# Kernel tuning notes

Hardware: AMD Instinct MI355X
Metric: run time of the kernel (lower is better)

Reference implementation:

```python
import jax, jax.numpy as jnp
import numpy as np

T, H = 4096, 2048

def setup_inputs() -> dict:
    key = jax.random.key(0)
    k1, k2, k3 = jax.random.split(key, 3)
    x_sequence = jax.random.normal(k1, (T, H), dtype=jnp.float32)
    lamda = jax.random.normal(k2, (H,), dtype=jnp.float32) * 0.2
    B = jax.random.normal(k3, (H, H), dtype=jnp.float32) / jnp.sqrt(jnp.float32(H))
    return {"x_sequence": x_sequence, "lamda": lamda, "B": B}

def reference(x_sequence, lamda, B):
    # h_t = lamda \odot h_{t-1} + B @ x_t ; initial h_0 = 0 (reset_rtrl_state).
    # Returns stacked h over all T steps, matching torch.stack(outputs).
    def step(h, x_t):
        h_next = lamda * h + B @ x_t  # [H]
        return h_next, h_next
    h0 = jnp.zeros_like(lamda)
    _, hs = jax.lax.scan(step, h0, x_sequence)  # hs: [T, H]
    return hs
```

## Files before the change

kernel.cpp:

```cpp
#include <hip/hip_runtime.h>
#include <hip/hip_bf16.h>

#define T_DIM 4096
#define H_DIM 2048
#define K_DIM 2048
#define NCHUNK 64
#define CLEN 64
#define NT (K_DIM / 64)

typedef float f32x4 __attribute__((ext_vector_type(4)));
typedef _Float16 f16x8 __attribute__((ext_vector_type(8)));

typedef const __attribute__((address_space(1))) char* gp1;
typedef __attribute__((address_space(3))) char* lp3;

static const size_t nX = (size_t)T_DIM * K_DIM;
static const size_t nB = (size_t)H_DIM * K_DIM;

__global__ __launch_bounds__(256) void cvt_swz_all(const float* __restrict__ X,
                                                   const float* __restrict__ Bm,
                                                   _Float16* __restrict__ Xh,
                                                   _Float16* __restrict__ Bh) {
    size_t i = ((size_t)blockIdx.x * 256 + threadIdx.x) * 8;
    const float* in;
    _Float16* out;
    size_t j;
    if (i < nX) { in = X;  out = Xh; j = i; }
    else        { in = Bm; out = Bh; j = i - nX; }
    int row  = (int)(j >> 11);
    int colB = (int)(j & 2047) * 2;
    float a[8];
    *(f32x4*)(a)     = *(const f32x4*)(in + j);
    *(f32x4*)(a + 4) = *(const f32x4*)(in + j + 4);
    f16x8 h;
#pragma unroll
    for (int k = 0; k < 8; ++k) h[k] = (_Float16)a[k];
    size_t ob = (size_t)row * 4096 + (size_t)(colB ^ ((row & 7) << 4));
    *(f16x8*)((char*)out + ob) = h;
}

__global__ __launch_bounds__(512) void gemm_f16(const _Float16* __restrict__ Xh,
                                                const _Float16* __restrict__ Bh,
                                                const float* __restrict__ lamda,
                                                float* __restrict__ Y,
                                                float* __restrict__ e) {
    __shared__ __align__(16) _Float16 sA[2][128 * 64];
    __shared__ __align__(16) _Float16 sB[2][128 * 64];

    int bid = blockIdx.x;
    int swz = (bid & 7) * 64 + (bid >> 3);
    const int h0 = (swz & 15) * 128;
    const int t0 = (swz >> 4) * 128;

    const int tid  = threadIdx.x;
    const int lane = tid & 63;
    const int wave = tid >> 6;
    const int wrow = wave >> 2;
    const int wcol = wave & 3;
    const int ln15 = lane & 15;
    const int kq   = lane >> 4;

    f32x4 acc[4][2] = {};

    const int srow = tid >> 3;
    const int kcB  = (tid & 7) * 16;
    size_t gA0[2], gB0[2];
    unsigned ldsOff[2];
#pragma unroll
    for (int q = 0; q < 2; ++q) {
        gA0[q] = (size_t)(t0 + srow + q * 64) * 4096 + kcB;
        gB0[q] = (size_t)(h0 + srow + q * 64) * 4096 + kcB;
        ldsOff[q] = (unsigned)((q * 512 + wave * 64) * 16);
    }

    int baseA[4], swzA[4], baseB[2], swzB[2];
#pragma unroll
    for (int m = 0; m < 4; ++m) {
        int rA = wrow * 64 + m * 16 + ln15;
        baseA[m] = rA * 128; swzA[m] = (rA & 7) << 4;
    }
#pragma unroll
    for (int n = 0; n < 2; ++n) {
        int rB = wcol * 32 + n * 16 + ln15;
        baseB[n] = rB * 128; swzB[n] = (rB & 7) << 4;
    }

#define STAGE(buf, kt)                                                                   \
    {                                                                                    \
        _Pragma("unroll")                                                                \
        for (int q = 0; q < 2; ++q) {                                                    \
            __builtin_amdgcn_global_load_lds((gp1)((const char*)Xh + gA0[q] + (kt) * 128), \
                                             (lp3)((char*)sA[buf] + ldsOff[q]), 16, 0, 0); \
            __builtin_amdgcn_global_load_lds((gp1)((const char*)Bh + gB0[q] + (kt) * 128), \
                                             (lp3)((char*)sB[buf] + ldsOff[q]), 16, 0, 0); \
        }                                                                                \
    }

#define COMPUTE(buf)                                                                     \
    {                                                                                    \
        const char* pA = (const char*)sA[buf];                                           \
        const char* pB = (const char*)sB[buf];                                           \
        _Pragma("unroll")                                                                \
        for (int kk = 0; kk < 2; ++kk) {                                                 \
            const int kb = kk * 64 + kq * 16;                                            \
            f16x8 fa[4], fb[2];                                                          \
            _Pragma("unroll")                                                            \
            for (int m = 0; m < 4; ++m)                                                  \
                fa[m] = *(const f16x8*)(pA + baseA[m] + (kb ^ swzA[m]));                 \
            _Pragma("unroll")                                                            \
            for (int n = 0; n < 2; ++n)                                                  \
                fb[n] = *(const f16x8*)(pB + baseB[n] + (kb ^ swzB[n]));                 \
            _Pragma("unroll")                                                            \
            for (int m = 0; m < 4; ++m)                                                  \
                _Pragma("unroll")                                                        \
                for (int n = 0; n < 2; ++n)                                              \
                    acc[m][n] = __builtin_amdgcn_mfma_f32_16x16x32_f16(fa[m], fb[n],     \
                                                                      acc[m][n], 0, 0, 0); \
        }                                                                                \
    }

    STAGE(0, 0);
    __syncthreads();

    int cur = 0;
    for (int kt = 0; kt < NT; ++kt) {
        if (kt + 1 < NT) STAGE(cur ^ 1, kt + 1);
        COMPUTE(cur);
        __syncthreads();
        cur ^= 1;
    }
#undef STAGE
#undef COMPUTE

#pragma unroll
    for (int m = 0; m < 4; ++m) {
        int row = t0 + wrow * 64 + m * 16 + kq * 4;
#pragma unroll
        for (int n = 0; n < 2; ++n) {
            int col = h0 + wcol * 32 + n * 16 + ln15;
#pragma unroll
            for (int j = 0; j < 4; ++j)
                Y[(size_t)(row + j) * H_DIM + col] = acc[m][n][j];
        }
    }

    const int c = (t0 >> 6) + wrow;
#pragma unroll
    for (int n = 0; n < 2; ++n) {
        int col = h0 + wcol * 32 + n * 16 + ln15;
        float lam  = lamda[col];
        float lam2 = lam * lam;
        float lam4 = lam2 * lam2;
        float lam16 = lam4 * lam4 * lam4 * lam4;
        float hsum = 0.f;
#pragma unroll
        for (int m = 0; m < 4; ++m) {
            float hm = fmaf(fmaf(fmaf(acc[m][n][0], lam, acc[m][n][1]), lam,
                                 acc[m][n][2]), lam, acc[m][n][3]);
            hsum = fmaf(hsum, lam16, hm);
        }
        float w = 1.f;
        if (kq < 3) w = lam4;
        if (kq < 2) w *= lam4;
        if (kq < 1) w *= lam4;
        float T = hsum * w;
        T += __shfl_xor(T, 16);
        T += __shfl_xor(T, 32);
        if (kq == 0) e[(size_t)c * H_DIM + col] = T;
    }
}

__global__ __launch_bounds__(256) void scanCB(float* __restrict__ Y,
                                              const float* __restrict__ lamda,
                                              const float* __restrict__ e) {
    int c = blockIdx.x >> 3;
    int h = (blockIdx.x & 7) * 256 + threadIdx.x;
    float lam = lamda[h];
    float lamL = lam;
#pragma unroll
    for (int i = 0; i < 6; ++i) lamL *= lamL;
    float s = 0.f;
    for (int ci = 0; ci < c; ++ci)
        s = fmaf(lamL, s, e[(size_t)ci * H_DIM + h]);
    float* q = Y + (size_t)c * CLEN * H_DIM + h;
#pragma unroll
    for (int t = 0; t < CLEN; ++t) {
        float v = fmaf(lam, s, q[(size_t)t * H_DIM]);
        q[(size_t)t * H_DIM] = v;
        s = v;
    }
}

__global__ __launch_bounds__(256) void gemm_xbT_split(const float* __restrict__ X,
                                                      const float* __restrict__ Bm,
                                                      float* __restrict__ Y) {
    __shared__ __align__(16) _Float16 Ah[128 * 64];
    __shared__ __align__(16) _Float16 Al[128 * 64];
    __shared__ __align__(16) _Float16 Bh2[128 * 64];
    __shared__ __align__(16) _Float16 Bl[128 * 64];

    const int tid  = threadIdx.x;
    const int t0   = blockIdx.y * 128;
    const int h0   = blockIdx.x * 128;
    const int lane = tid & 63;
    const int wave = tid >> 6;
    const int wrow = wave >> 1;
    const int wcol = wave & 1;
    const int ln15 = lane & 15;
    const int kq   = lane >> 4;

    f32x4 acc[4][4] = {};

    int baseA[4], swzA[4], baseB[4], swzB[4];
#pragma unroll
    for (int m = 0; m < 4; ++m) {
        int rA = wrow * 64 + m * 16 + ln15;
        baseA[m] = rA * 128; swzA[m] = (rA & 7) << 4;
        int rB = wcol * 64 + m * 16 + ln15;
        baseB[m] = rB * 128; swzB[m] = (rB & 7) << 4;
    }

    for (int kt = 0; kt < NT; ++kt) {
        const int k0 = kt * 64;
        __syncthreads();
#pragma unroll
        for (int t = 0; t < 4; ++t) {
            int c   = tid + t * 256;
            int row = c >> 3;
            int kc  = (c & 7) * 8;
            size_t gA = (size_t)(t0 + row) * K_DIM + k0 + kc;
            size_t gB = (size_t)(h0 + row) * K_DIM + k0 + kc;
            float a[8], b[8];
            *(float4*)(a)     = *(const float4*)(X + gA);
            *(float4*)(a + 4) = *(const float4*)(X + gA + 4);
            *(float4*)(b)     = *(const float4*)(Bm + gB);
            *(float4*)(b + 4) = *(const float4*)(Bm + gB + 4);
            f16x8 ah, al, bh, bl;
#pragma unroll
            for (int j = 0; j < 8; ++j) {
                _Float16 hh = (_Float16)a[j];
                ah[j] = hh; al[j] = (_Float16)(a[j] - (float)hh);
                _Float16 gg = (_Float16)b[j];
                bh[j] = gg; bl[j] = (_Float16)(b[j] - (float)gg);
            }
            int off = row * 128 + ((kc * 2) ^ ((row & 7) << 4));
            *(f16x8*)((char*)Ah + off)  = ah;
            *(f16x8*)((char*)Al + off)  = al;
            *(f16x8*)((char*)Bh2 + off) = bh;
            *(f16x8*)((char*)Bl + off)  = bl;
        }
        __syncthreads();
#pragma unroll
        for (int kk = 0; kk < 2; ++kk) {
            const int kb = kk * 64 + kq * 16;
            f16x8 fa[4], fb[4], ft[4];
#pragma unroll
            for (int m = 0; m < 4; ++m)
                fa[m] = *(const f16x8*)((const char*)Ah + baseA[m] + (kb ^ swzA[m]));
#pragma unroll
            for (int m = 0; m < 4; ++m)
                fb[m] = *(const f16x8*)((const char*)Bh2 + baseB[m] + (kb ^ swzB[m]));
#pragma unroll
            for (int m = 0; m < 4; ++m)
#pragma unroll
                for (int n = 0; n < 4; ++n)
                    acc[m][n] = __builtin_amdgcn_mfma_f32_16x16x32_f16(fa[m], fb[n], acc[m][n], 0, 0, 0);
#pragma unroll
            for (int m = 0; m < 4; ++m)
                ft[m] = *(const f16x8*)((const char*)Bl + baseB[m] + (kb ^ swzB[m]));
#pragma unroll
            for (int m = 0; m < 4; ++m)
#pragma unroll
                for (int n = 0; n < 4; ++n)
                    acc[m][n] = __builtin_amdgcn_mfma_f32_16x16x32_f16(fa[m], ft[n], acc[m][n], 0, 0, 0);
#pragma unroll
            for (int m = 0; m < 4; ++m)
                ft[m] = *(const f16x8*)((const char*)Al + baseA[m] + (kb ^ swzA[m]));
#pragma unroll
            for (int m = 0; m < 4; ++m)
#pragma unroll
                for (int n = 0; n < 4; ++n)
                    acc[m][n] = __builtin_amdgcn_mfma_f32_16x16x32_f16(ft[m], fb[n], acc[m][n], 0, 0, 0);
        }
    }

#pragma unroll
    for (int m = 0; m < 4; ++m) {
        int row = t0 + wrow * 64 + m * 16 + kq * 4;
#pragma unroll
        for (int n = 0; n < 4; ++n) {
            int col = h0 + wcol * 64 + n * 16 + ln15;
#pragma unroll
            for (int j = 0; j < 4; ++j)
                Y[(size_t)(row + j) * H_DIM + col] = acc[m][n][j];
        }
    }
}

__global__ __launch_bounds__(256) void scanA(const float* __restrict__ Y,
                                             const float* __restrict__ lamda,
                                             float* __restrict__ e) {
    int c = blockIdx.x >> 3;
    int h = (blockIdx.x & 7) * 256 + threadIdx.x;
    float lam = lamda[h];
    float s = 0.f;
    const float* p = Y + (size_t)c * CLEN * H_DIM + h;
#pragma unroll
    for (int t = 0; t < CLEN; ++t) { s = fmaf(lam, s, *p); p += H_DIM; }
    e[(size_t)c * H_DIM + h] = s;
}

extern "C" void kernel_launch(void* const* d_in, const int* in_sizes, int n_in,
                              void* d_out, int out_size, void* d_ws, size_t ws_size,
                              hipStream_t stream) {
    const float* X   = (const float*)d_in[0];
    const float* lam = (const float*)d_in[1];
    const float* Bm  = (const float*)d_in[2];
    float* Y = (float*)d_out;

    const size_t needFused = (nX + nB) * sizeof(_Float16)
                           + (size_t)NCHUNK * H_DIM * sizeof(float);

    if (ws_size >= needFused) {
        _Float16* Xh = (_Float16*)d_ws;
        _Float16* Bh = Xh + nX;
        float* e = (float*)(Bh + nB);

        int cvtBlocks = (int)((nX + nB) / 8 / 256);
        cvt_swz_all<<<dim3(cvtBlocks), 256, 0, stream>>>(X, Bm, Xh, Bh);
        gemm_f16<<<dim3(512), 512, 0, stream>>>(Xh, Bh, lam, Y, e);
        scanCB<<<dim3(NCHUNK * 8), 256, 0, stream>>>(Y, lam, e);
    } else {
        dim3 grid(H_DIM / 128, T_DIM / 128);
        gemm_xbT_split<<<grid, 256, 0, stream>>>(X, Bm, Y);
        float* e = (float*)d_ws;
        scanA<<<dim3(NCHUNK * 8), 256, 0, stream>>>(Y, lam, e);
        scanCB<<<dim3(NCHUNK * 8), 256, 0, stream>>>(Y, lam, e);
    }
}
```

Before: 77.23 us.

## Split K across wave pairs with 64x64 warp tiles and LDS reduction

The GEMM's 8 waves are reorganised from a 2x4 grid of 64x32 output tiles into a 2x2 grid of 64x64 tiles, with the two waves of each pair splitting the 128-wide K slice of every stage. Each wave now loads 8 fragments per 16 MFMAs instead of 12 per 16, which cuts LDS read traffic per MFMA. At the end the partial accumulators are summed through shared memory, reusing the staging buffers, before the Y and chunk-carry epilogue runs. The cost is twice as many accumulator registers per wave, an extra barrier and reduction pass, and only half the waves doing the epilogue. A minimum-blocks hint of 4 is added to launch bounds.

```diff
diff --git a/kernel.cpp b/kernel.cpp
--- a/kernel.cpp
+++ b/kernel.cpp
@@ -39,13 +39,12 @@
     *(f16x8*)((char*)out + ob) = h;
 }
 
-__global__ __launch_bounds__(512) void gemm_f16(const _Float16* __restrict__ Xh,
-                                                const _Float16* __restrict__ Bh,
-                                                const float* __restrict__ lamda,
-                                                float* __restrict__ Y,
-                                                float* __restrict__ e) {
-    __shared__ __align__(16) _Float16 sA[2][128 * 64];
-    __shared__ __align__(16) _Float16 sB[2][128 * 64];
+__global__ __launch_bounds__(512, 4) void gemm_f16(const _Float16* __restrict__ Xh,
+                                                   const _Float16* __restrict__ Bh,
+                                                   const float* __restrict__ lamda,
+                                                   float* __restrict__ Y,
+                                                   float* __restrict__ e) {
+    __shared__ __align__(16) _Float16 sMem[2][2][128 * 64];
 
     int bid = blockIdx.x;
     int swz = (bid & 7) * 64 + (bid >> 3);
@@ -55,12 +54,13 @@
     const int tid  = threadIdx.x;
     const int lane = tid & 63;
     const int wave = tid >> 6;
-    const int wrow = wave >> 2;
-    const int wcol = wave & 3;
+    const int wrow = (wave >> 2) & 1;
+    const int wcol = (wave >> 1) & 1;
+    const int kks  = wave & 1;
     const int ln15 = lane & 15;
     const int kq   = lane >> 4;
 
-    f32x4 acc[4][2] = {};
+    f32x4 acc[4][4] = {};
 
     const int srow = tid >> 3;
     const int kcB  = (tid & 7) * 16;
@@ -70,19 +70,17 @@
     for (int q = 0; q < 2; ++q) {
         gA0[q] = (size_t)(t0 + srow + q * 64) * 4096 + kcB;
         gB0[q] = (size_t)(h0 + srow + q * 64) * 4096 + kcB;
-        ldsOff[q] = (unsigned)((q * 512 + wave * 64) * 16);
-    }
-
-    int baseA[4], swzA[4], baseB[2], swzB[2];
+        ldsOff[q] = (unsigned)(q * 8192 + wave * 1024);
+    }
+
+    const int kb = kks * 64 + kq * 16;
+    int offA[4], offB[4];
 #pragma unroll
     for (int m = 0; m < 4; ++m) {
         int rA = wrow * 64 + m * 16 + ln15;
-        baseA[m] = rA * 128; swzA[m] = (rA & 7) << 4;
-    }
-#pragma unroll
-    for (int n = 0; n < 2; ++n) {
-        int rB = wcol * 32 + n * 16 + ln15;
-        baseB[n] = rB * 128; swzB[n] = (rB & 7) << 4;
+        offA[m] = rA * 128 + (kb ^ ((rA & 7) << 4));
+        int rB = wcol * 64 + m * 16 + ln15;
+        offB[m] = rB * 128 + (kb ^ ((rB & 7) << 4));
     }
 
 #define STAGE(buf, kt)                                                                   \
@@ -90,33 +88,27 @@
         _Pragma("unroll")                                                                \
         for (int q = 0; q < 2; ++q) {                                                    \
             __builtin_amdgcn_global_load_lds((gp1)((const char*)Xh + gA0[q] + (kt) * 128), \
-                                             (lp3)((char*)sA[buf] + ldsOff[q]), 16, 0, 0); \
+                                             (lp3)((char*)sMem[buf][0] + ldsOff[q]), 16, 0, 0); \
             __builtin_amdgcn_global_load_lds((gp1)((const char*)Bh + gB0[q] + (kt) * 128), \
-                                             (lp3)((char*)sB[buf] + ldsOff[q]), 16, 0, 0); \
+                                             (lp3)((char*)sMem[buf][1] + ldsOff[q]), 16, 0, 0); \
         }                                                                                \
     }
 
 #define COMPUTE(buf)                                                                     \
     {                                                                                    \
-        const char* pA = (const char*)sA[buf];                                           \
-        const char* pB = (const char*)sB[buf];                                           \
+        const char* pA = (const char*)sMem[buf][0];                                      \
+        const char* pB = (const char*)sMem[buf][1];                                      \
+        f16x8 fa[4], fb[4];                                                              \
         _Pragma("unroll")                                                                \
-        for (int kk = 0; kk < 2; ++kk) {                                                 \
-            const int kb = kk * 64 + kq * 16;                                            \
-            f16x8 fa[4], fb[2];                                                          \
+        for (int m = 0; m < 4; ++m) fa[m] = *(const f16x8*)(pA + offA[m]);               \
+        _Pragma("unroll")                                                                \
+        for (int n = 0; n < 4; ++n) fb[n] = *(const f16x8*)(pB + offB[n]);               \
+        _Pragma("unroll")                                                                \
+        for (int m = 0; m < 4; ++m)                                                      \
             _Pragma("unroll")                                                            \
-            for (int m = 0; m < 4; ++m)                                                  \
-                fa[m] = *(const f16x8*)(pA + baseA[m] + (kb ^ swzA[m]));                 \
-            _Pragma("unroll")                                                            \
-            for (int n = 0; n < 2; ++n)                                                  \
-                fb[n] = *(const f16x8*)(pB + baseB[n] + (kb ^ swzB[n]));                 \
-            _Pragma("unroll")                                                            \
-            for (int m = 0; m < 4; ++m)                                                  \
-                _Pragma("unroll")                                                        \
-                for (int n = 0; n < 2; ++n)                                              \
-                    acc[m][n] = __builtin_amdgcn_mfma_f32_16x16x32_f16(fa[m], fb[n],     \
-                                                                      acc[m][n], 0, 0, 0); \
-        }                                                                                \
+            for (int n = 0; n < 4; ++n)                                                  \
+                acc[m][n] = __builtin_amdgcn_mfma_f32_16x16x32_f16(fa[m], fb[n],         \
+                                                                  acc[m][n], 0, 0, 0);  \
     }
 
     STAGE(0, 0);
@@ -132,41 +124,59 @@
 #undef STAGE
 #undef COMPUTE
 
-#pragma unroll
-    for (int m = 0; m < 4; ++m) {
-        int row = t0 + wrow * 64 + m * 16 + kq * 4;
-#pragma unroll
-        for (int n = 0; n < 2; ++n) {
-            int col = h0 + wcol * 32 + n * 16 + ln15;
-#pragma unroll
-            for (int j = 0; j < 4; ++j)
-                Y[(size_t)(row + j) * H_DIM + col] = acc[m][n][j];
-        }
-    }
-
-    const int c = (t0 >> 6) + wrow;
-#pragma unroll
-    for (int n = 0; n < 2; ++n) {
-        int col = h0 + wcol * 32 + n * 16 + ln15;
-        float lam  = lamda[col];
-        float lam2 = lam * lam;
-        float lam4 = lam2 * lam2;
-        float lam16 = lam4 * lam4 * lam4 * lam4;
-        float hsum = 0.f;
+    const int p = wrow * 2 + wcol;
+    float* red = (float*)sMem;
+    if (kks == 1) {
+#pragma unroll
+        for (int m = 0; m < 4; ++m)
+#pragma unroll
+            for (int n = 0; n < 4; ++n)
+                *(f32x4*)((char*)red + p * 16384 + (m * 4 + n) * 1024 + lane * 16) = acc[m][n];
+    }
+    __syncthreads();
+    if (kks == 0) {
+#pragma unroll
+        for (int m = 0; m < 4; ++m)
+#pragma unroll
+            for (int n = 0; n < 4; ++n)
+                acc[m][n] += *(const f32x4*)((const char*)red + p * 16384 + (m * 4 + n) * 1024 + lane * 16);
+
 #pragma unroll
         for (int m = 0; m < 4; ++m) {
-            float hm = fmaf(fmaf(fmaf(acc[m][n][0], lam, acc[m][n][1]), lam,
-                                 acc[m][n][2]), lam, acc[m][n][3]);
-            hsum = fmaf(hsum, lam16, hm);
-        }
-        float w = 1.f;
-        if (kq < 3) w = lam4;
-        if (kq < 2) w *= lam4;
-        if (kq < 1) w *= lam4;
-        float T = hsum * w;
-        T += __shfl_xor(T, 16);
-        T += __shfl_xor(T, 32);
-        if (kq == 0) e[(size_t)c * H_DIM + col] = T;
+            int row = t0 + wrow * 64 + m * 16 + kq * 4;
+#pragma unroll
+            for (int n = 0; n < 4; ++n) {
+                int col = h0 + wcol * 64 + n * 16 + ln15;
+#pragma unroll
+                for (int j = 0; j < 4; ++j)
+                    Y[(size_t)(row + j) * H_DIM + col] = acc[m][n][j];
+            }
+        }
+
+        const int c = (t0 >> 6) + wrow;
+#pragma unroll
+        for (int n = 0; n < 4; ++n) {
+            int col = h0 + wcol * 64 + n * 16 + ln15;
+            float lam  = lamda[col];
+            float lam2 = lam * lam;
+            float lam4 = lam2 * lam2;
+            float lam16 = lam4 * lam4 * lam4 * lam4;
+            float hsum = 0.f;
+#pragma unroll
+            for (int m = 0; m < 4; ++m) {
+                float hm = fmaf(fmaf(fmaf(acc[m][n][0], lam, acc[m][n][1]), lam,
+                                     acc[m][n][2]), lam, acc[m][n][3]);
+                hsum = fmaf(hsum, lam16, hm);
+            }
+            float w = 1.f;
+            if (kq < 3) w = lam4;
+            if (kq < 2) w *= lam4;
+            if (kq < 1) w *= lam4;
+            float T = hsum * w;
+            T += __shfl_xor(T, 16);
+            T += __shfl_xor(T, 32);
+            if (kq == 0) e[(size_t)c * H_DIM + col] = T;
+        }
     }
 }
 
```

Result: no change. 76.45 us (-1.0%).
